# Kernel optimization log

Measured on AMD Instinct MI355X. Metric: run time of the kernel, lower is better.

The kernel has to match this reference:

```python
import jax, jax.numpy as jnp
import numpy as np

B, N, D, H_IMG, W_IMG = 1, 6, 128, 28, 60
HB, WB = 50, 50
HEADS, DH = 4, 32
INNER = HEADS * DH  # 128 == D
Q = HB * WB
NK = N * H_IMG * W_IMG


def _ln(x, w, b, eps=1e-5):
    m = jnp.mean(x, axis=-1, keepdims=True)
    v = jnp.var(x, axis=-1, keepdims=True)
    return (x - m) * jax.lax.rsqrt(v + eps) * w + b


def setup_inputs() -> dict:
    key = jax.random.key(0)
    ks = jax.random.split(key, 20)
    s = 0.02
    inp = {
        "q": jax.random.normal(ks[0], (B, D, HB, WB), jnp.float32),
        "k": jax.random.normal(ks[1], (B, N, D, H_IMG, W_IMG), jnp.float32),
        "v": jax.random.normal(ks[2], (B, N, D, H_IMG, W_IMG), jnp.float32),
        "W_logits": jax.random.uniform(ks[3], (B, Q, NK), jnp.float32),
        "vis_flat": jax.random.randint(ks[4], (B, Q, NK), 0, 2).astype(jnp.int32),
        "skip": jax.random.normal(ks[5], (B, D, HB, WB), jnp.float32),
        # LayerNorm params
        "qn_w": jnp.ones((D,), jnp.float32), "qn_b": jnp.zeros((D,), jnp.float32),
        "kn_w": jnp.ones((D,), jnp.float32), "kn_b": jnp.zeros((D,), jnp.float32),
        "vn_w": jnp.ones((D,), jnp.float32), "vn_b": jnp.zeros((D,), jnp.float32),
        "pre_w": jnp.ones((D,), jnp.float32), "pre_b": jnp.zeros((D,), jnp.float32),
        "post_w": jnp.ones((D,), jnp.float32), "post_b": jnp.zeros((D,), jnp.float32),
        # Linear params, stored [in, out]
        "wq": jax.random.normal(ks[6], (D, INNER), jnp.float32) * s,
        "bq": jnp.zeros((INNER,), jnp.float32),
        "wk": jax.random.normal(ks[7], (D, INNER), jnp.float32) * s,
        "bk": jnp.zeros((INNER,), jnp.float32),
        "wv": jax.random.normal(ks[8], (D, INNER), jnp.float32) * s,
        "bv": jnp.zeros((INNER,), jnp.float32),
        "wp": jax.random.normal(ks[9], (INNER, D), jnp.float32) * s,
        "bp": jnp.zeros((D,), jnp.float32),
        "w1": jax.random.normal(ks[10], (D, 2 * D), jnp.float32) * s,
        "b1": jnp.zeros((2 * D,), jnp.float32),
        "w2": jax.random.normal(ks[11], (2 * D, D), jnp.float32) * s,
        "b2": jnp.zeros((D,), jnp.float32),
    }
    return inp


def reference(q, k, v, W_logits, vis_flat, skip,
              qn_w, qn_b, kn_w, kn_b, vn_w, vn_b, pre_w, pre_b, post_w, post_b,
              wq, bq, wk, bk, wv, bv, wp, bp, w1, b1, w2, b2):
    b, d, Hb, Wb = q.shape
    _, n, _, hi, wi = k.shape
    Qn = Hb * Wb
    # b d H W -> b (H W) d ; b n d h w -> b (n h w) d
    qf = q.reshape(b, d, Qn).transpose(0, 2, 1)
    kf = k.transpose(0, 1, 3, 4, 2).reshape(b, n * hi * wi, d)
    vf = v.transpose(0, 1, 3, 4, 2).reshape(b, n * hi * wi, d)
    qf = _ln(qf, qn_w, qn_b)
    kf = _ln(kf, kn_w, kn_b)
    vf = _ln(vf, vn_w, vn_b)
    qh = (qf @ wq + bq).reshape(b, Qn, HEADS, DH).transpose(0, 2, 1, 3)
    kh = (kf @ wk + bk).reshape(b, -1, HEADS, DH).transpose(0, 2, 1, 3)
    vh = (vf @ wv + bv).reshape(b, -1, HEADS, DH).transpose(0, 2, 1, 3)
    scale = DH ** (-0.5)
    logits = jnp.einsum('bhqd,bhkd->bhqk', qh, kh) * scale  # [b,h,Q,NK]
    neg_inf = jnp.finfo(logits.dtype).min
    logits = jnp.where(vis_flat[:, None] == 0, neg_inf, logits)
    logits = logits * W_logits[:, None]  # multiplicative EAF weighting
    attn = jax.nn.softmax(logits, axis=-1)
    out = jnp.einsum('bhqk,bhkd->bhqd', attn, vh)
    out = out.transpose(0, 2, 1, 3).reshape(b, Qn, INNER)
    out = out @ wp + bp
    z = out + skip.reshape(b, d, Qn).transpose(0, 2, 1)
    z = _ln(z, pre_w, pre_b)
    z = z + (jax.nn.gelu(z @ w1 + b1, approximate=False) @ w2 + b2)
    z = _ln(z, post_w, post_b)
    return z.transpose(0, 2, 1).reshape(b, d, Hb, Wb)
```

## Files before the change

### kernel.cpp

```cpp
#include <hip/hip_runtime.h>
#include <hip/hip_bf16.h>
#include <math.h>

typedef short short8 __attribute__((ext_vector_type(8)));
typedef float floatx4 __attribute__((ext_vector_type(4)));

#define D 128
#define Q 2500
#define QPAD 2560
#define NK 10080
#define NKPAD 10112
#define QSCALE 0.25501268426834347f
#define NEGBIG -3.0e38f

__device__ __forceinline__ unsigned short f2bf(float f) {
    unsigned u = __float_as_uint(f);
    unsigned r = (u + 0x7fffu + ((u >> 16) & 1u)) >> 16;
    return (unsigned short)r;
}

__global__ void ln_kernel(const float* __restrict__ qi, const float* __restrict__ ki,
                          const float* __restrict__ vi,
                          const float* __restrict__ qw, const float* __restrict__ qb,
                          const float* __restrict__ kw, const float* __restrict__ kb,
                          const float* __restrict__ vw, const float* __restrict__ vb,
                          unsigned short* __restrict__ xq, unsigned short* __restrict__ xk,
                          unsigned short* __restrict__ xv) {
    int job = blockIdx.x * 4 + (threadIdx.x >> 6);
    int lane = threadIdx.x & 63;
    const float *g, *b, *a0, *a1;
    unsigned short* dst;
    if (job < Q) {
        int p = job;
        a0 = qi + lane * Q + p; a1 = qi + (lane + 64) * Q + p;
        g = qw; b = qb; dst = xq + p * D;
    } else if (job < Q + NK) {
        int p = job - Q;
        int n = p / 1680; int r = p - n * 1680;
        const float* base = ki + (n * 128) * 1680 + r;
        a0 = base + lane * 1680; a1 = base + (lane + 64) * 1680;
        g = kw; b = kb; dst = xk + p * D;
    } else {
        int p = job - (Q + NK);
        int n = p / 1680; int r = p - n * 1680;
        const float* base = vi + (n * 128) * 1680 + r;
        a0 = base + lane * 1680; a1 = base + (lane + 64) * 1680;
        g = vw; b = vb; dst = xv + p * D;
    }
    float x0 = *a0, x1 = *a1;
    float s = x0 + x1, ss = x0 * x0 + x1 * x1;
    #pragma unroll
    for (int m = 1; m <= 32; m <<= 1) {
        s += __shfl_xor(s, m, 64);
        ss += __shfl_xor(ss, m, 64);
    }
    float mean = s * (1.0f / 128.0f);
    float var = ss * (1.0f / 128.0f) - mean * mean;
    float rstd = rsqrtf(var + 1e-5f);
    dst[lane] = f2bf((x0 - mean) * rstd * g[lane] + b[lane]);
    dst[lane + 64] = f2bf((x1 - mean) * rstd * g[lane + 64] + b[lane + 64]);
}

__global__ __launch_bounds__(256) void proj_kernel(
    const unsigned short* __restrict__ xq, const unsigned short* __restrict__ xk,
    const unsigned short* __restrict__ xv,
    const float* __restrict__ wq, const float* __restrict__ bq,
    const float* __restrict__ wk, const float* __restrict__ bk,
    const float* __restrict__ wv, const float* __restrict__ bv,
    unsigned short* __restrict__ qh, unsigned short* __restrict__ kh,
    unsigned short* __restrict__ vh) {
    int bid = blockIdx.x;
    const unsigned short* src; const float *w, *bias; unsigned short* dst; float scale; int mb;
    if (bid < 40)       { src = xq; w = wq; bias = bq; dst = qh; scale = QSCALE; mb = bid * 64; }
    else if (bid < 198) { src = xk; w = wk; bias = bk; dst = kh; scale = 1.0f;  mb = (bid - 40) * 64; }
    else                { src = xv; w = wv; bias = bv; dst = vh; scale = 1.0f;  mb = (bid - 198) * 64; }
    int wave = threadIdx.x >> 6, lane = threadIdx.x & 63;
    int l15 = lane & 15, quad = lane >> 4;
    int m0 = mb + wave * 16;
    floatx4 acc[8];
    #pragma unroll
    for (int i = 0; i < 8; i++) acc[i] = (floatx4){0.f, 0.f, 0.f, 0.f};
    #pragma unroll
    for (int kf = 0; kf < 4; kf++) {
        short8 A = *(const short8*)(src + (m0 + l15) * D + kf * 32 + quad * 8);
        #pragma unroll
        for (int nt = 0; nt < 8; nt++) {
            short8 B;
            #pragma unroll
            for (int j = 0; j < 8; j++)
                B[j] = (short)f2bf(w[(kf * 32 + quad * 8 + j) * D + nt * 16 + l15]);
            acc[nt] = __builtin_amdgcn_mfma_f32_16x16x32_bf16(A, B, acc[nt], 0, 0, 0);
        }
    }
    #pragma unroll
    for (int nt = 0; nt < 8; nt++) {
        float bb = bias[nt * 16 + l15];
        #pragma unroll
        for (int r = 0; r < 4; r++)
            dst[(m0 + quad * 4 + r) * D + nt * 16 + l15] = f2bf((acc[nt][r] + bb) * scale);
    }
}

__global__ __launch_bounds__(256) void attn_kernel(
    const unsigned short* __restrict__ qh, const unsigned short* __restrict__ kh,
    const unsigned short* __restrict__ vh,
    const float* __restrict__ Wl, const int* __restrict__ vis,
    float* __restrict__ Opart, float* __restrict__ lpart) {
    __shared__ short plds[4 * 2 * 16 * 40];
    int bid = blockIdx.x;
    int split = bid & 7, qt = bid >> 3;
    int h = threadIdx.x >> 6, lane = threadIdx.x & 63;
    int l15 = lane & 15, quad = lane >> 4;
    int qb = qt * 32;
    int kb0 = split * 1280;
    int nch = (split == 7) ? 35 : 40;
    short* pw = plds + h * 1280;

    short8 qA[2];
    #pragma unroll
    for (int s = 0; s < 2; s++)
        qA[s] = *(const short8*)(qh + (qb + s * 16 + l15) * D + h * 32 + quad * 8);

    const float* wrow[8]; const int* vrow[8];
    #pragma unroll
    for (int s = 0; s < 2; s++)
        #pragma unroll
        for (int r = 0; r < 4; r++) {
            int row = qb + s * 16 + quad * 4 + r;
            row = row < Q ? row : (Q - 1);
            wrow[s * 4 + r] = Wl + (size_t)row * NK;
            vrow[s * 4 + r] = vis + (size_t)row * NK;
        }

    const floatx4 zf = {0.f, 0.f, 0.f, 0.f};
    floatx4 O[2][2];
    float lacc[2][4];
    #pragma unroll
    for (int s = 0; s < 2; s++)
        #pragma unroll
        for (int i = 0; i < 4; i++) { lacc[s][i] = 0.f; }
    O[0][0] = zf; O[0][1] = zf; O[1][0] = zf; O[1][1] = zf;

    for (int c = 0; c < nch; c++) {
        int kb = kb0 + c * 32;
        short8 kB0 = *(const short8*)(kh + (kb + l15) * D + h * 32 + quad * 8);
        short8 kB1 = *(const short8*)(kh + (kb + 16 + l15) * D + h * 32 + quad * 8);
        short8 vB0, vB1;
        #pragma unroll
        for (int j = 0; j < 8; j++) {
            int kk = kb + quad * 8 + j;
            vB0[j] = (short)vh[kk * D + h * 32 + l15];
            vB1[j] = (short)vh[kk * D + h * 32 + 16 + l15];
        }
        #pragma unroll
        for (int s = 0; s < 2; s++) {
            floatx4 S0 = __builtin_amdgcn_mfma_f32_16x16x32_bf16(qA[s], kB0, zf, 0, 0, 0);
            floatx4 S1 = __builtin_amdgcn_mfma_f32_16x16x32_bf16(qA[s], kB1, zf, 0, 0, 0);
            #pragma unroll
            for (int r = 0; r < 4; r++) {
                const float* wr = wrow[s * 4 + r];
                const int* vr = vrow[s * 4 + r];
                float w0 = wr[kb + l15], w1 = wr[kb + 16 + l15];
                int v0 = vr[kb + l15], v1 = vr[kb + 16 + l15];
                float L0 = (v0 ? S0[r] : NEGBIG) * w0;
                float L1 = (v1 ? S1[r] : NEGBIG) * w1;
                float p0 = exp2f(L0), p1 = exp2f(L1);
                lacc[s][r] += p0 + p1;
                pw[s * 640 + (quad * 4 + r) * 40 + l15] = (short)f2bf(p0);
                pw[s * 640 + (quad * 4 + r) * 40 + 16 + l15] = (short)f2bf(p1);
            }
        }
        #pragma unroll
        for (int s = 0; s < 2; s++) {
            short8 P = *(const short8*)(pw + s * 640 + l15 * 40 + quad * 8);
            O[s][0] = __builtin_amdgcn_mfma_f32_16x16x32_bf16(P, vB0, O[s][0], 0, 0, 0);
            O[s][1] = __builtin_amdgcn_mfma_f32_16x16x32_bf16(P, vB1, O[s][1], 0, 0, 0);
        }
    }

    #pragma unroll
    for (int s = 0; s < 2; s++)
        #pragma unroll
        for (int r = 0; r < 4; r++) {
            float lv = lacc[s][r];
            lv += __shfl_xor(lv, 1, 64);
            lv += __shfl_xor(lv, 2, 64);
            lv += __shfl_xor(lv, 4, 64);
            lv += __shfl_xor(lv, 8, 64);
            int row = qb + s * 16 + quad * 4 + r;
            if (l15 == 0) lpart[(split * QPAD + row) * 4 + h] = lv;
            float* op = Opart + ((size_t)(split * QPAD + row) * 4 + h) * 32;
            op[l15] = O[s][0][r];
            op[16 + l15] = O[s][1][r];
        }
}

__global__ __launch_bounds__(256) void epi_kernel(
    const float* __restrict__ Opart, const float* __restrict__ lpart,
    const float* __restrict__ wp, const float* __restrict__ bp,
    const float* __restrict__ skip,
    const float* __restrict__ pre_w, const float* __restrict__ pre_b,
    const float* __restrict__ w1, const float* __restrict__ b1,
    const float* __restrict__ w2, const float* __restrict__ b2,
    const float* __restrict__ post_w, const float* __restrict__ post_b,
    float* __restrict__ out) {
    __shared__ __align__(16) char smem[68608];
    short* A1 = (short*)smem;
    short* Z1 = (short*)(smem + 17408);
    short* H1 = (short*)(smem + 34816);
    float* Zout = (float*)smem;

    int qb = blockIdx.x * 64;
    int t = threadIdx.x;
    int wave = t >> 6, lane = t & 63;
    int l15 = lane & 15, quad = lane >> 4;
    int m0 = wave * 16;

    {
        int pl = t >> 2, hh = t & 3;
        int q = qb + pl;
        if (q < Q) {
            float ltot = 0.f;
            #pragma unroll
            for (int s = 0; s < 8; s++) ltot += lpart[(s * QPAD + q) * 4 + hh];
            float inv = 1.0f / fmaxf(ltot, 1e-30f);
            floatx4 acc4[8];
            #pragma unroll
            for (int i = 0; i < 8; i++) acc4[i] = (floatx4){0.f, 0.f, 0.f, 0.f};
            #pragma unroll
            for (int s = 0; s < 8; s++) {
                const floatx4* op = (const floatx4*)(Opart + ((size_t)(s * QPAD + q) * 4 + hh) * 32);
                #pragma unroll
                for (int i = 0; i < 8; i++) acc4[i] += op[i];
            }
            #pragma unroll
            for (int i = 0; i < 8; i++)
                #pragma unroll
                for (int j = 0; j < 4; j++)
                    A1[pl * 136 + hh * 32 + i * 4 + j] = (short)f2bf(acc4[i][j] * inv);
        } else {
            #pragma unroll
            for (int d = 0; d < 32; d++) A1[pl * 136 + hh * 32 + d] = 0;
        }
    }

    floatx4 z[8];
    #pragma unroll
    for (int i = 0; i < 8; i++) z[i] = (floatx4){0.f, 0.f, 0.f, 0.f};
    #pragma unroll
    for (int kf = 0; kf < 4; kf++) {
        short8 A = *(const short8*)(A1 + (m0 + l15) * 136 + kf * 32 + quad * 8);
        #pragma unroll
        for (int nt = 0; nt < 8; nt++) {
            short8 B;
            #pragma unroll
            for (int j = 0; j < 8; j++)
                B[j] = (short)f2bf(wp[(kf * 32 + quad * 8 + j) * D + nt * 16 + l15]);
            z[nt] = __builtin_amdgcn_mfma_f32_16x16x32_bf16(A, B, z[nt], 0, 0, 0);
        }
    }
    float Zv[8][4];
    #pragma unroll
    for (int nt = 0; nt < 8; nt++) {
        int n = nt * 16 + l15;
        float bb = bp[n];
        #pragma unroll
        for (int r = 0; r < 4; r++) {
            int q = qb + m0 + quad * 4 + r;
            int qc = q < Q ? q : (Q - 1);
            Zv[nt][r] = z[nt][r] + bb + skip[n * Q + qc];
        }
    }
    float Zn[8][4];
    {
        #pragma unroll
        for (int r = 0; r < 4; r++) {
            float s1 = 0.f, s2 = 0.f;
            #pragma unroll
            for (int nt = 0; nt < 8; nt++) { s1 += Zv[nt][r]; s2 += Zv[nt][r] * Zv[nt][r]; }
            s1 += __shfl_xor(s1, 1, 64); s2 += __shfl_xor(s2, 1, 64);
            s1 += __shfl_xor(s1, 2, 64); s2 += __shfl_xor(s2, 2, 64);
            s1 += __shfl_xor(s1, 4, 64); s2 += __shfl_xor(s2, 4, 64);
            s1 += __shfl_xor(s1, 8, 64); s2 += __shfl_xor(s2, 8, 64);
            float mean = s1 * (1.0f / 128.0f);
            float var = s2 * (1.0f / 128.0f) - mean * mean;
            float rstd = rsqrtf(var + 1e-5f);
            #pragma unroll
            for (int nt = 0; nt < 8; nt++) Zn[nt][r] = (Zv[nt][r] - mean) * rstd;
        }
        #pragma unroll
        for (int nt = 0; nt < 8; nt++) {
            int n = nt * 16 + l15;
            float g = pre_w[n], be = pre_b[n];
            #pragma unroll
            for (int r = 0; r < 4; r++) {
                Zn[nt][r] = Zn[nt][r] * g + be;
                Z1[(m0 + quad * 4 + r) * 136 + n] = (short)f2bf(Zn[nt][r]);
            }
        }
    }
    {
        floatx4 h2[16];
        #pragma unroll
        for (int i = 0; i < 16; i++) h2[i] = (floatx4){0.f, 0.f, 0.f, 0.f};
        #pragma unroll
        for (int kf = 0; kf < 4; kf++) {
            short8 A = *(const short8*)(Z1 + (m0 + l15) * 136 + kf * 32 + quad * 8);
            #pragma unroll
            for (int nt = 0; nt < 16; nt++) {
                short8 B;
                #pragma unroll
                for (int j = 0; j < 8; j++)
                    B[j] = (short)f2bf(w1[(kf * 32 + quad * 8 + j) * 256 + nt * 16 + l15]);
                h2[nt] = __builtin_amdgcn_mfma_f32_16x16x32_bf16(A, B, h2[nt], 0, 0, 0);
            }
        }
        #pragma unroll
        for (int nt = 0; nt < 16; nt++) {
            int n = nt * 16 + l15;
            float bb = b1[n];
            #pragma unroll
            for (int r = 0; r < 4; r++) {
                float x = h2[nt][r] + bb;
                float gl = 0.5f * x * (1.0f + erff(x * 0.70710678118654752f));
                H1[(m0 + quad * 4 + r) * 264 + n] = (short)f2bf(gl);
            }
        }
    }
    floatx4 o3[8];
    #pragma unroll
    for (int i = 0; i < 8; i++) o3[i] = (floatx4){0.f, 0.f, 0.f, 0.f};
    #pragma unroll
    for (int kf = 0; kf < 8; kf++) {
        short8 A = *(const short8*)(H1 + (m0 + l15) * 264 + kf * 32 + quad * 8);
        #pragma unroll
        for (int nt = 0; nt < 8; nt++) {
            short8 B;
            #pragma unroll
            for (int j = 0; j < 8; j++)
                B[j] = (short)f2bf(w2[(kf * 32 + quad * 8 + j) * D + nt * 16 + l15]);
            o3[nt] = __builtin_amdgcn_mfma_f32_16x16x32_bf16(A, B, o3[nt], 0, 0, 0);
        }
    }
    float Z2[8][4];
    #pragma unroll
    for (int nt = 0; nt < 8; nt++) {
        int n = nt * 16 + l15;
        float bb = b2[n];
        #pragma unroll
        for (int r = 0; r < 4; r++) Z2[nt][r] = Zn[nt][r] + o3[nt][r] + bb;
    }
    float Zo[8][4];
    {
        #pragma unroll
        for (int r = 0; r < 4; r++) {
            float s1 = 0.f, s2 = 0.f;
            #pragma unroll
            for (int nt = 0; nt < 8; nt++) { s1 += Z2[nt][r]; s2 += Z2[nt][r] * Z2[nt][r]; }
            s1 += __shfl_xor(s1, 1, 64); s2 += __shfl_xor(s2, 1, 64);
            s1 += __shfl_xor(s1, 2, 64); s2 += __shfl_xor(s2, 2, 64);
            s1 += __shfl_xor(s1, 4, 64); s2 += __shfl_xor(s2, 4, 64);
            s1 += __shfl_xor(s1, 8, 64); s2 += __shfl_xor(s2, 8, 64);
            float mean = s1 * (1.0f / 128.0f);
            float var = s2 * (1.0f / 128.0f) - mean * mean;
            float rstd = rsqrtf(var + 1e-5f);
            #pragma unroll
            for (int nt = 0; nt < 8; nt++) Zo[nt][r] = (Z2[nt][r] - mean) * rstd;
        }
        #pragma unroll
        for (int nt = 0; nt < 8; nt++) {
            int n = nt * 16 + l15;
            float g = post_w[n], be = post_b[n];
            #pragma unroll
            for (int r = 0; r < 4; r++) Zo[nt][r] = Zo[nt][r] * g + be;
        }
    }
    __syncthreads();
    #pragma unroll
    for (int nt = 0; nt < 8; nt++)
        #pragma unroll
        for (int r = 0; r < 4; r++)
            Zout[(nt * 16 + l15) * 65 + m0 + quad * 4 + r] = Zo[nt][r];
    __syncthreads();
    {
        int pl = t & 63;
        int q = qb + pl;
        if (q < Q) {
            #pragma unroll
            for (int it = 0; it < 32; it++) {
                int n = it * 4 + (t >> 6);
                out[n * Q + q] = Zout[n * 65 + pl];
            }
        }
    }
}

extern "C" void kernel_launch(void* const* d_in, const int* in_sizes, int n_in,
                              void* d_out, int out_size, void* d_ws, size_t ws_size,
                              hipStream_t stream) {
    (void)in_sizes; (void)n_in; (void)out_size; (void)ws_size;
    const float* q      = (const float*)d_in[0];
    const float* k      = (const float*)d_in[1];
    const float* v      = (const float*)d_in[2];
    const float* Wl     = (const float*)d_in[3];
    const int*   vis    = (const int*)  d_in[4];
    const float* skip   = (const float*)d_in[5];
    const float* qn_w   = (const float*)d_in[6];
    const float* qn_b   = (const float*)d_in[7];
    const float* kn_w   = (const float*)d_in[8];
    const float* kn_b   = (const float*)d_in[9];
    const float* vn_w   = (const float*)d_in[10];
    const float* vn_b   = (const float*)d_in[11];
    const float* pre_w  = (const float*)d_in[12];
    const float* pre_b  = (const float*)d_in[13];
    const float* post_w = (const float*)d_in[14];
    const float* post_b = (const float*)d_in[15];
    const float* wq     = (const float*)d_in[16];
    const float* bq     = (const float*)d_in[17];
    const float* wk     = (const float*)d_in[18];
    const float* bk     = (const float*)d_in[19];
    const float* wv     = (const float*)d_in[20];
    const float* bv     = (const float*)d_in[21];
    const float* wp     = (const float*)d_in[22];
    const float* bp     = (const float*)d_in[23];
    const float* w1     = (const float*)d_in[24];
    const float* b1     = (const float*)d_in[25];
    const float* w2     = (const float*)d_in[26];
    const float* b2     = (const float*)d_in[27];
    float* out = (float*)d_out;

    char* ws = (char*)d_ws;
    unsigned short* xq = (unsigned short*)(ws + 0);
    unsigned short* xk = (unsigned short*)(ws + 655360);
    unsigned short* xv = (unsigned short*)(ws + 3244032);
    unsigned short* qh = (unsigned short*)(ws + 5832704);
    unsigned short* kh = (unsigned short*)(ws + 6488064);
    unsigned short* vh = (unsigned short*)(ws + 9076736);
    float* Opart = (float*)(ws + 11665408);
    float* lpart = (float*)(ws + 22151168);

    ln_kernel<<<dim3(5665), dim3(256), 0, stream>>>(q, k, v, qn_w, qn_b, kn_w, kn_b, vn_w, vn_b,
                                                    xq, xk, xv);
    proj_kernel<<<dim3(356), dim3(256), 0, stream>>>(xq, xk, xv, wq, bq, wk, bk, wv, bv,
                                                     qh, kh, vh);
    attn_kernel<<<dim3(632), dim3(256), 0, stream>>>(qh, kh, vh, Wl, vis, Opart, lpart);
    epi_kernel<<<dim3(40), dim3(256), 0, stream>>>(Opart, lpart, wp, bp, skip,
                                                   pre_w, pre_b, w1, b1, w2, b2,
                                                   post_w, post_b, out);
}
```

Baseline: 433.8 us.

## Restructure pipeline: pre-transposed bf16 weights, all-heads attention waves, more splits

A new kernel converts and transposes all weights to bf16 once, so the GEMMs load B fragments as vectors instead of gathering and converting scalars. LayerNorm is rewritten to stage tiles in LDS so global loads are coalesced. V is stored transposed so attention reads it as vectors. Attention now has each wave cover all four heads for 16 queries, which reuses the Wl/vis loads across heads, and the key range is split 35 ways for more blocks. The old epilogue becomes separate linv, combine and MLP kernels, which adds launches and a larger partial-output buffer.

```diff
diff --git a/kernel.cpp b/kernel.cpp
--- a/kernel.cpp
+++ b/kernel.cpp
@@ -10,6 +10,8 @@
 #define QPAD 2560
 #define NK 10080
 #define NKPAD 10112
+#define SPLITS 35
+#define CPS 9
 #define QSCALE 0.25501268426834347f
 #define NEGBIG -3.0e38f
 
@@ -18,63 +20,121 @@
     unsigned r = (u + 0x7fffu + ((u >> 16) & 1u)) >> 16;
     return (unsigned short)r;
 }
-
-__global__ void ln_kernel(const float* __restrict__ qi, const float* __restrict__ ki,
-                          const float* __restrict__ vi,
-                          const float* __restrict__ qw, const float* __restrict__ qb,
-                          const float* __restrict__ kw, const float* __restrict__ kb,
-                          const float* __restrict__ vw, const float* __restrict__ vb,
-                          unsigned short* __restrict__ xq, unsigned short* __restrict__ xk,
-                          unsigned short* __restrict__ xv) {
-    int job = blockIdx.x * 4 + (threadIdx.x >> 6);
-    int lane = threadIdx.x & 63;
-    const float *g, *b, *a0, *a1;
-    unsigned short* dst;
-    if (job < Q) {
-        int p = job;
-        a0 = qi + lane * Q + p; a1 = qi + (lane + 64) * Q + p;
-        g = qw; b = qb; dst = xq + p * D;
-    } else if (job < Q + NK) {
-        int p = job - Q;
-        int n = p / 1680; int r = p - n * 1680;
-        const float* base = ki + (n * 128) * 1680 + r;
-        a0 = base + lane * 1680; a1 = base + (lane + 64) * 1680;
-        g = kw; b = kb; dst = xk + p * D;
+__device__ __forceinline__ unsigned pack2bf(float lo, float hi) {
+    unsigned u0 = __float_as_uint(lo) + 0x8000u;
+    unsigned u1 = __float_as_uint(hi) + 0x8000u;
+    return (u0 >> 16) | (u1 & 0xffff0000u);
+}
+__device__ __forceinline__ float bflo(unsigned u) { return __uint_as_float(u << 16); }
+__device__ __forceinline__ float bfhi(unsigned u) { return __uint_as_float(u & 0xffff0000u); }
+
+__global__ void wcvt_kernel(const float* __restrict__ wq, const float* __restrict__ wk,
+                            const float* __restrict__ wv, const float* __restrict__ wp,
+                            const float* __restrict__ w1, const float* __restrict__ w2,
+                            unsigned short* __restrict__ wqT, unsigned short* __restrict__ wkT,
+                            unsigned short* __restrict__ wvT, unsigned short* __restrict__ wpT,
+                            unsigned short* __restrict__ w1T, unsigned short* __restrict__ w2T) {
+    int idx = blockIdx.x * 256 + threadIdx.x;
+    if (idx < 49152) {
+        int m = idx >> 14;
+        int local = idx & 16383;
+        int n = local >> 7, kk = local & 127;
+        const float* w = (m == 0) ? wq : ((m == 1) ? wk : wv);
+        unsigned short* o = (m == 0) ? wqT : ((m == 1) ? wkT : wvT);
+        o[local] = f2bf(w[kk * 128 + n]);
+    } else if (idx < 65536) {
+        int local = idx - 49152;
+        int n = local >> 7, kk = local & 127;
+        int b = kk >> 5, j = kk & 31;
+        int ko = b * 32 + ((j & 1) ? 16 + (j >> 1) : (j >> 1));
+        wpT[local] = f2bf(wp[ko * 128 + n]);
+    } else if (idx < 98304) {
+        int local = idx - 65536;
+        int n = local >> 7, kk = local & 127;
+        w1T[local] = f2bf(w1[kk * 256 + n]);
     } else {
-        int p = job - (Q + NK);
-        int n = p / 1680; int r = p - n * 1680;
-        const float* base = vi + (n * 128) * 1680 + r;
-        a0 = base + lane * 1680; a1 = base + (lane + 64) * 1680;
-        g = vw; b = vb; dst = xv + p * D;
-    }
-    float x0 = *a0, x1 = *a1;
-    float s = x0 + x1, ss = x0 * x0 + x1 * x1;
-    #pragma unroll
-    for (int m = 1; m <= 32; m <<= 1) {
-        s += __shfl_xor(s, m, 64);
-        ss += __shfl_xor(ss, m, 64);
-    }
+        int local = idx - 98304;
+        int n = local >> 8, kk = local & 255;
+        w2T[local] = f2bf(w2[kk * 128 + n]);
+    }
+}
+
+__global__ __launch_bounds__(256) void ln_kernel(
+    const float* __restrict__ qi, const float* __restrict__ ki, const float* __restrict__ vi,
+    const float* __restrict__ qw, const float* __restrict__ qb,
+    const float* __restrict__ kw, const float* __restrict__ kb,
+    const float* __restrict__ vw, const float* __restrict__ vb,
+    unsigned short* __restrict__ xq, unsigned short* __restrict__ xk,
+    unsigned short* __restrict__ xv) {
+    __shared__ float lds[16 * 132];
+    int bid = blockIdx.x, t = threadIdx.x;
+    const float* src; unsigned short* dst; const float *g, *b;
+    int S, valid;
+    if (bid < 157) {
+        int p0 = bid * 16;
+        src = qi + p0; S = Q; dst = xq + p0 * D; g = qw; b = qb;
+        valid = Q - p0; if (valid > 16) valid = 16;
+    } else if (bid < 787) {
+        int tt = bid - 157;
+        int n = tt / 105, r = (tt - n * 105) * 16;
+        src = ki + (size_t)(n * 128) * 1680 + r; S = 1680;
+        dst = xk + (n * 1680 + r) * D; g = kw; b = kb; valid = 16;
+    } else {
+        int tt = bid - 787;
+        int n = tt / 105, r = (tt - n * 105) * 16;
+        src = vi + (size_t)(n * 128) * 1680 + r; S = 1680;
+        dst = xv + (n * 1680 + r) * D; g = vw; b = vb; valid = 16;
+    }
+    int c4 = t & 3, d = t >> 2;
+    floatx4 fa = {0.f, 0.f, 0.f, 0.f}, fb = {0.f, 0.f, 0.f, 0.f};
+    if (c4 * 4 < valid) {
+        fa = *(const floatx4*)(src + d * S + c4 * 4);
+        fb = *(const floatx4*)(src + (d + 64) * S + c4 * 4);
+    }
+    #pragma unroll
+    for (int j = 0; j < 4; j++) {
+        lds[(c4 * 4 + j) * 132 + d] = fa[j];
+        lds[(c4 * 4 + j) * 132 + d + 64] = fb[j];
+    }
+    __syncthreads();
+    int lane = t & 63, wv = t >> 6;
+    int pos = wv * 4 + (lane >> 4), l15 = lane & 15;
+    floatx4 xa = *(const floatx4*)(&lds[pos * 132 + l15 * 8]);
+    floatx4 xb = *(const floatx4*)(&lds[pos * 132 + l15 * 8 + 4]);
+    float s = 0.f, ss = 0.f;
+    #pragma unroll
+    for (int j = 0; j < 4; j++) { s += xa[j] + xb[j]; ss += xa[j] * xa[j] + xb[j] * xb[j]; }
+    #pragma unroll
+    for (int m = 1; m <= 8; m <<= 1) { s += __shfl_xor(s, m, 64); ss += __shfl_xor(ss, m, 64); }
     float mean = s * (1.0f / 128.0f);
     float var = ss * (1.0f / 128.0f) - mean * mean;
     float rstd = rsqrtf(var + 1e-5f);
-    dst[lane] = f2bf((x0 - mean) * rstd * g[lane] + b[lane]);
-    dst[lane + 64] = f2bf((x1 - mean) * rstd * g[lane + 64] + b[lane + 64]);
+    floatx4 g0 = *(const floatx4*)(g + l15 * 8), g1 = *(const floatx4*)(g + l15 * 8 + 4);
+    floatx4 b0 = *(const floatx4*)(b + l15 * 8), b1 = *(const floatx4*)(b + l15 * 8 + 4);
+    short8 o;
+    #pragma unroll
+    for (int j = 0; j < 4; j++) {
+        o[j] = (short)f2bf((xa[j] - mean) * rstd * g0[j] + b0[j]);
+        o[4 + j] = (short)f2bf((xb[j] - mean) * rstd * g1[j] + b1[j]);
+    }
+    if (pos < valid) *(short8*)(dst + pos * D + l15 * 8) = o;
 }
 
 __global__ __launch_bounds__(256) void proj_kernel(
     const unsigned short* __restrict__ xq, const unsigned short* __restrict__ xk,
     const unsigned short* __restrict__ xv,
-    const float* __restrict__ wq, const float* __restrict__ bq,
-    const float* __restrict__ wk, const float* __restrict__ bk,
-    const float* __restrict__ wv, const float* __restrict__ bv,
+    const unsigned short* __restrict__ wqT, const unsigned short* __restrict__ wkT,
+    const unsigned short* __restrict__ wvT,
+    const float* __restrict__ bq, const float* __restrict__ bk, const float* __restrict__ bv,
     unsigned short* __restrict__ qh, unsigned short* __restrict__ kh,
-    unsigned short* __restrict__ vh) {
+    unsigned short* __restrict__ vhT) {
+    __shared__ short vlds[128 * 72];
     int bid = blockIdx.x;
-    const unsigned short* src; const float *w, *bias; unsigned short* dst; float scale; int mb;
-    if (bid < 40)       { src = xq; w = wq; bias = bq; dst = qh; scale = QSCALE; mb = bid * 64; }
-    else if (bid < 198) { src = xk; w = wk; bias = bk; dst = kh; scale = 1.0f;  mb = (bid - 40) * 64; }
-    else                { src = xv; w = wv; bias = bv; dst = vh; scale = 1.0f;  mb = (bid - 198) * 64; }
-    int wave = threadIdx.x >> 6, lane = threadIdx.x & 63;
+    const unsigned short *src, *wT; const float* bias; int mb, mode; float scale;
+    if (bid < 40)       { mode = 0; src = xq; wT = wqT; bias = bq; mb = bid * 64; scale = QSCALE; }
+    else if (bid < 198) { mode = 1; src = xk; wT = wkT; bias = bk; mb = (bid - 40) * 64; scale = 1.0f; }
+    else                { mode = 2; src = xv; wT = wvT; bias = bv; mb = (bid - 198) * 64; scale = 1.0f; }
+    int t = threadIdx.x, wave = t >> 6, lane = t & 63;
     int l15 = lane & 15, quad = lane >> 4;
     int m0 = mb + wave * 16;
     floatx4 acc[8];
@@ -85,178 +145,183 @@
         short8 A = *(const short8*)(src + (m0 + l15) * D + kf * 32 + quad * 8);
         #pragma unroll
         for (int nt = 0; nt < 8; nt++) {
-            short8 B;
-            #pragma unroll
-            for (int j = 0; j < 8; j++)
-                B[j] = (short)f2bf(w[(kf * 32 + quad * 8 + j) * D + nt * 16 + l15]);
-            acc[nt] = __builtin_amdgcn_mfma_f32_16x16x32_bf16(A, B, acc[nt], 0, 0, 0);
-        }
-    }
-    #pragma unroll
-    for (int nt = 0; nt < 8; nt++) {
-        float bb = bias[nt * 16 + l15];
-        #pragma unroll
-        for (int r = 0; r < 4; r++)
-            dst[(m0 + quad * 4 + r) * D + nt * 16 + l15] = f2bf((acc[nt][r] + bb) * scale);
+            short8 Bv = *(const short8*)(wT + (nt * 16 + l15) * D + kf * 32 + quad * 8);
+            acc[nt] = __builtin_amdgcn_mfma_f32_16x16x32_bf16(A, Bv, acc[nt], 0, 0, 0);
+        }
+    }
+    if (mode != 2) {
+        unsigned short* dst = (mode == 0) ? qh : kh;
+        #pragma unroll
+        for (int nt = 0; nt < 8; nt++) {
+            float bb = bias[nt * 16 + l15];
+            #pragma unroll
+            for (int r = 0; r < 4; r++)
+                dst[(m0 + quad * 4 + r) * D + nt * 16 + l15] = f2bf((acc[nt][r] + bb) * scale);
+        }
+    } else {
+        #pragma unroll
+        for (int nt = 0; nt < 8; nt++) {
+            float bb = bias[nt * 16 + l15];
+            #pragma unroll
+            for (int r = 0; r < 4; r++)
+                vlds[(nt * 16 + l15) * 72 + (wave * 16 + quad * 4 + r)] =
+                    (short)f2bf(acc[nt][r] + bb);
+        }
+        __syncthreads();
+        int pr = t & 31, dd = t >> 5;
+        int sub = pr >> 4, i = pr & 15;
+        #pragma unroll
+        for (int pass = 0; pass < 16; pass++) {
+            int d = pass * 8 + dd;
+            unsigned lo = (unsigned short)vlds[d * 72 + sub * 32 + i];
+            unsigned hi = (unsigned short)vlds[d * 72 + sub * 32 + 16 + i];
+            *(unsigned*)(vhT + (size_t)d * NKPAD + mb + sub * 32 + 2 * i) = lo | (hi << 16);
+        }
     }
 }
 
 __global__ __launch_bounds__(256) void attn_kernel(
     const unsigned short* __restrict__ qh, const unsigned short* __restrict__ kh,
-    const unsigned short* __restrict__ vh,
+    const unsigned short* __restrict__ vhT,
     const float* __restrict__ Wl, const int* __restrict__ vis,
-    float* __restrict__ Opart, float* __restrict__ lpart) {
-    __shared__ short plds[4 * 2 * 16 * 40];
+    unsigned* __restrict__ OpartU, float* __restrict__ lpart) {
+    __shared__ unsigned pP[4 * 4 * 16 * 20];
     int bid = blockIdx.x;
-    int split = bid & 7, qt = bid >> 3;
-    int h = threadIdx.x >> 6, lane = threadIdx.x & 63;
+    int split = bid % SPLITS, qt = bid / SPLITS;
+    int t = threadIdx.x, wave = t >> 6, lane = t & 63;
     int l15 = lane & 15, quad = lane >> 4;
-    int qb = qt * 32;
-    int kb0 = split * 1280;
-    int nch = (split == 7) ? 35 : 40;
-    short* pw = plds + h * 1280;
-
-    short8 qA[2];
-    #pragma unroll
-    for (int s = 0; s < 2; s++)
-        qA[s] = *(const short8*)(qh + (qb + s * 16 + l15) * D + h * 32 + quad * 8);
-
-    const float* wrow[8]; const int* vrow[8];
-    #pragma unroll
-    for (int s = 0; s < 2; s++)
+    int qb = qt * 64 + wave * 16;
+    int k00 = split * (CPS * 32);
+    unsigned* pw = pP + wave * 1280;
+
+    short8 qA[4];
+    #pragma unroll
+    for (int h = 0; h < 4; h++)
+        qA[h] = *(const short8*)(qh + (qb + l15) * D + h * 32 + quad * 8);
+
+    const float* wrow[4]; const int* vrow[4];
+    #pragma unroll
+    for (int r = 0; r < 4; r++) {
+        int row = qb + quad * 4 + r;
+        row = row < Q ? row : (Q - 1);
+        wrow[r] = Wl + (size_t)row * NK;
+        vrow[r] = vis + (size_t)row * NK;
+    }
+
+    const floatx4 zf = {0.f, 0.f, 0.f, 0.f};
+    floatx4 O[4][2];
+    float lacc[4][4];
+    #pragma unroll
+    for (int h = 0; h < 4; h++) {
+        O[h][0] = zf; O[h][1] = zf;
+        #pragma unroll
+        for (int r = 0; r < 4; r++) lacc[h][r] = 0.f;
+    }
+
+    #pragma unroll 1
+    for (int c = 0; c < CPS; c++) {
+        int k0 = k00 + c * 32;
+        float w0[4], w1[4]; int msk0[4], msk1[4];
         #pragma unroll
         for (int r = 0; r < 4; r++) {
-            int row = qb + s * 16 + quad * 4 + r;
-            row = row < Q ? row : (Q - 1);
-            wrow[s * 4 + r] = Wl + (size_t)row * NK;
-            vrow[s * 4 + r] = vis + (size_t)row * NK;
-        }
-
-    const floatx4 zf = {0.f, 0.f, 0.f, 0.f};
-    floatx4 O[2][2];
-    float lacc[2][4];
-    #pragma unroll
-    for (int s = 0; s < 2; s++)
-        #pragma unroll
-        for (int i = 0; i < 4; i++) { lacc[s][i] = 0.f; }
-    O[0][0] = zf; O[0][1] = zf; O[1][0] = zf; O[1][1] = zf;
-
-    for (int c = 0; c < nch; c++) {
-        int kb = kb0 + c * 32;
-        short8 kB0 = *(const short8*)(kh + (kb + l15) * D + h * 32 + quad * 8);
-        short8 kB1 = *(const short8*)(kh + (kb + 16 + l15) * D + h * 32 + quad * 8);
-        short8 vB0, vB1;
-        #pragma unroll
-        for (int j = 0; j < 8; j++) {
-            int kk = kb + quad * 8 + j;
-            vB0[j] = (short)vh[kk * D + h * 32 + l15];
-            vB1[j] = (short)vh[kk * D + h * 32 + 16 + l15];
-        }
-        #pragma unroll
-        for (int s = 0; s < 2; s++) {
-            floatx4 S0 = __builtin_amdgcn_mfma_f32_16x16x32_bf16(qA[s], kB0, zf, 0, 0, 0);
-            floatx4 S1 = __builtin_amdgcn_mfma_f32_16x16x32_bf16(qA[s], kB1, zf, 0, 0, 0);
+            w0[r] = wrow[r][k0 + l15];
+            w1[r] = wrow[r][k0 + 16 + l15];
+            msk0[r] = vrow[r][k0 + l15];
+            msk1[r] = vrow[r][k0 + 16 + l15];
+        }
+        #pragma unroll
+        for (int h = 0; h < 4; h++) {
+            short8 kB0 = *(const short8*)(kh + (k0 + l15) * D + h * 32 + quad * 8);
+            short8 kB1 = *(const short8*)(kh + (k0 + 16 + l15) * D + h * 32 + quad * 8);
+            floatx4 S0 = __builtin_amdgcn_mfma_f32_16x16x32_bf16(qA[h], kB0, zf, 0, 0, 0);
+            floatx4 S1 = __builtin_amdgcn_mfma_f32_16x16x32_bf16(qA[h], kB1, zf, 0, 0, 0);
             #pragma unroll
             for (int r = 0; r < 4; r++) {
-                const float* wr = wrow[s * 4 + r];
-                const int* vr = vrow[s * 4 + r];
-                float w0 = wr[kb + l15], w1 = wr[kb + 16 + l15];
-                int v0 = vr[kb + l15], v1 = vr[kb + 16 + l15];
-                float L0 = (v0 ? S0[r] : NEGBIG) * w0;
-                float L1 = (v1 ? S1[r] : NEGBIG) * w1;
+                float L0 = (msk0[r] ? S0[r] : NEGBIG) * w0[r];
+                float L1 = (msk1[r] ? S1[r] : NEGBIG) * w1[r];
                 float p0 = exp2f(L0), p1 = exp2f(L1);
-                lacc[s][r] += p0 + p1;
-                pw[s * 640 + (quad * 4 + r) * 40 + l15] = (short)f2bf(p0);
-                pw[s * 640 + (quad * 4 + r) * 40 + 16 + l15] = (short)f2bf(p1);
+                lacc[h][r] += p0 + p1;
+                pw[h * 320 + (quad * 4 + r) * 20 + l15] = pack2bf(p0, p1);
             }
         }
         #pragma unroll
-        for (int s = 0; s < 2; s++) {
-            short8 P = *(const short8*)(pw + s * 640 + l15 * 40 + quad * 8);
-            O[s][0] = __builtin_amdgcn_mfma_f32_16x16x32_bf16(P, vB0, O[s][0], 0, 0, 0);
-            O[s][1] = __builtin_amdgcn_mfma_f32_16x16x32_bf16(P, vB1, O[s][1], 0, 0, 0);
-        }
-    }
-
-    #pragma unroll
-    for (int s = 0; s < 2; s++)
+        for (int h = 0; h < 4; h++) {
+            short8 P = *(const short8*)(pw + h * 320 + l15 * 20 + quad * 4);
+            short8 vB0 = *(const short8*)(vhT + (size_t)(h * 32 + l15) * NKPAD + k0 + quad * 8);
+            short8 vB1 = *(const short8*)(vhT + (size_t)(h * 32 + 16 + l15) * NKPAD + k0 + quad * 8);
+            O[h][0] = __builtin_amdgcn_mfma_f32_16x16x32_bf16(P, vB0, O[h][0], 0, 0, 0);
+            O[h][1] = __builtin_amdgcn_mfma_f32_16x16x32_bf16(P, vB1, O[h][1], 0, 0, 0);
+        }
+    }
+
+    #pragma unroll
+    for (int h = 0; h < 4; h++)
         #pragma unroll
         for (int r = 0; r < 4; r++) {
-            float lv = lacc[s][r];
+            float lv = lacc[h][r];
             lv += __shfl_xor(lv, 1, 64);
             lv += __shfl_xor(lv, 2, 64);
             lv += __shfl_xor(lv, 4, 64);
             lv += __shfl_xor(lv, 8, 64);
-            int row = qb + s * 16 + quad * 4 + r;
-            if (l15 == 0) lpart[(split * QPAD + row) * 4 + h] = lv;
-            float* op = Opart + ((size_t)(split * QPAD + row) * 4 + h) * 32;
-            op[l15] = O[s][0][r];
-            op[16 + l15] = O[s][1][r];
-        }
-}
-
-__global__ __launch_bounds__(256) void epi_kernel(
-    const float* __restrict__ Opart, const float* __restrict__ lpart,
-    const float* __restrict__ wp, const float* __restrict__ bp,
-    const float* __restrict__ skip,
+            int row = qb + quad * 4 + r;
+            int base = (split * QPAD + row) * 4 + h;
+            if (l15 == 0) lpart[base] = lv;
+            OpartU[base * 16 + l15] = pack2bf(O[h][0][r], O[h][1][r]);
+        }
+}
+
+__global__ void linv_kernel(const float* __restrict__ lpart, float* __restrict__ linv) {
+    int i = blockIdx.x * 256 + threadIdx.x;
+    float s = 0.f;
+    #pragma unroll 1
+    for (int sp = 0; sp < SPLITS; sp++) s += lpart[sp * QPAD * 4 + i];
+    linv[i] = 1.0f / fmaxf(s, 1e-30f);
+}
+
+__global__ void combine_kernel(const unsigned* __restrict__ OpartU,
+                               const float* __restrict__ linv,
+                               unsigned* __restrict__ A1u) {
+    int idx = blockIdx.x * 256 + threadIdx.x;
+    float lo = 0.f, hi = 0.f;
+    #pragma unroll 1
+    for (int sp = 0; sp < SPLITS; sp++) {
+        unsigned u = OpartU[(size_t)sp * (QPAD * 64) + idx];
+        lo += bflo(u);
+        hi += bfhi(u);
+    }
+    int q = idx >> 6, t6 = idx & 63;
+    float inv = linv[q * 4 + (t6 >> 4)];
+    A1u[idx] = pack2bf(lo * inv, hi * inv);
+}
+
+__global__ __launch_bounds__(256) void mlp_kernel(
+    const unsigned short* __restrict__ A1s, const unsigned short* __restrict__ wpT,
+    const float* __restrict__ bp, const float* __restrict__ skip,
     const float* __restrict__ pre_w, const float* __restrict__ pre_b,
-    const float* __restrict__ w1, const float* __restrict__ b1,
-    const float* __restrict__ w2, const float* __restrict__ b2,
+    const unsigned short* __restrict__ w1T, const float* __restrict__ b1,
+    const unsigned short* __restrict__ w2T, const float* __restrict__ b2,
     const float* __restrict__ post_w, const float* __restrict__ post_b,
     float* __restrict__ out) {
-    __shared__ __align__(16) char smem[68608];
-    short* A1 = (short*)smem;
-    short* Z1 = (short*)(smem + 17408);
-    short* H1 = (short*)(smem + 34816);
+    __shared__ __align__(16) char smem[51200];
+    short* Z1 = (short*)smem;
+    short* H1 = (short*)(smem + 17408);
     float* Zout = (float*)smem;
 
     int qb = blockIdx.x * 64;
-    int t = threadIdx.x;
-    int wave = t >> 6, lane = t & 63;
+    int t = threadIdx.x, wave = t >> 6, lane = t & 63;
     int l15 = lane & 15, quad = lane >> 4;
     int m0 = wave * 16;
 
-    {
-        int pl = t >> 2, hh = t & 3;
-        int q = qb + pl;
-        if (q < Q) {
-            float ltot = 0.f;
-            #pragma unroll
-            for (int s = 0; s < 8; s++) ltot += lpart[(s * QPAD + q) * 4 + hh];
-            float inv = 1.0f / fmaxf(ltot, 1e-30f);
-            floatx4 acc4[8];
-            #pragma unroll
-            for (int i = 0; i < 8; i++) acc4[i] = (floatx4){0.f, 0.f, 0.f, 0.f};
-            #pragma unroll
-            for (int s = 0; s < 8; s++) {
-                const floatx4* op = (const floatx4*)(Opart + ((size_t)(s * QPAD + q) * 4 + hh) * 32);
-                #pragma unroll
-                for (int i = 0; i < 8; i++) acc4[i] += op[i];
-            }
-            #pragma unroll
-            for (int i = 0; i < 8; i++)
-                #pragma unroll
-                for (int j = 0; j < 4; j++)
-                    A1[pl * 136 + hh * 32 + i * 4 + j] = (short)f2bf(acc4[i][j] * inv);
-        } else {
-            #pragma unroll
-            for (int d = 0; d < 32; d++) A1[pl * 136 + hh * 32 + d] = 0;
-        }
-    }
-
     floatx4 z[8];
     #pragma unroll
     for (int i = 0; i < 8; i++) z[i] = (floatx4){0.f, 0.f, 0.f, 0.f};
     #pragma unroll
     for (int kf = 0; kf < 4; kf++) {
-        short8 A = *(const short8*)(A1 + (m0 + l15) * 136 + kf * 32 + quad * 8);
-        #pragma unroll
-        for (int nt = 0; nt < 8; nt++) {
-            short8 B;
-            #pragma unroll
-            for (int j = 0; j < 8; j++)
-                B[j] = (short)f2bf(wp[(kf * 32 + quad * 8 + j) * D + nt * 16 + l15]);
-            z[nt] = __builtin_amdgcn_mfma_f32_16x16x32_bf16(A, B, z[nt], 0, 0, 0);
+        short8 A = *(const short8*)(A1s + (qb + m0 + l15) * D + kf * 32 + quad * 8);
+        #pragma unroll
+        for (int nt = 0; nt < 8; nt++) {
+            short8 Bv = *(const short8*)(wpT + (nt * 16 + l15) * D + kf * 32 + quad * 8);
+            z[nt] = __builtin_amdgcn_mfma_f32_16x16x32_bf16(A, Bv, z[nt], 0, 0, 0);
         }
     }
     float Zv[8][4];
@@ -278,10 +343,8 @@
             float s1 = 0.f, s2 = 0.f;
             #pragma unroll
             for (int nt = 0; nt < 8; nt++) { s1 += Zv[nt][r]; s2 += Zv[nt][r] * Zv[nt][r]; }
-            s1 += __shfl_xor(s1, 1, 64); s2 += __shfl_xor(s2, 1, 64);
-            s1 += __shfl_xor(s1, 2, 64); s2 += __shfl_xor(s2, 2, 64);
-            s1 += __shfl_xor(s1, 4, 64); s2 += __shfl_xor(s2, 4, 64);
-            s1 += __shfl_xor(s1, 8, 64); s2 += __shfl_xor(s2, 8, 64);
+            #pragma unroll
+            for (int m = 1; m <= 8; m <<= 1) { s1 += __shfl_xor(s1, m, 64); s2 += __shfl_xor(s2, m, 64); }
             float mean = s1 * (1.0f / 128.0f);
             float var = s2 * (1.0f / 128.0f) - mean * mean;
             float rstd = rsqrtf(var + 1e-5f);
@@ -308,11 +371,8 @@
             short8 A = *(const short8*)(Z1 + (m0 + l15) * 136 + kf * 32 + quad * 8);
             #pragma unroll
             for (int nt = 0; nt < 16; nt++) {
-                short8 B;
-                #pragma unroll
-                for (int j = 0; j < 8; j++)
-                    B[j] = (short)f2bf(w1[(kf * 32 + quad * 8 + j) * 256 + nt * 16 + l15]);
-                h2[nt] = __builtin_amdgcn_mfma_f32_16x16x32_bf16(A, B, h2[nt], 0, 0, 0);
+                short8 Bv = *(const short8*)(w1T + (nt * 16 + l15) * D + kf * 32 + quad * 8);
+                h2[nt] = __builtin_amdgcn_mfma_f32_16x16x32_bf16(A, Bv, h2[nt], 0, 0, 0);
             }
         }
         #pragma unroll
@@ -335,11 +395,8 @@
         short8 A = *(const short8*)(H1 + (m0 + l15) * 264 + kf * 32 + quad * 8);
         #pragma unroll
         for (int nt = 0; nt < 8; nt++) {
-            short8 B;
-            #pragma unroll
-            for (int j = 0; j < 8; j++)
-                B[j] = (short)f2bf(w2[(kf * 32 + quad * 8 + j) * D + nt * 16 + l15]);
-            o3[nt] = __builtin_amdgcn_mfma_f32_16x16x32_bf16(A, B, o3[nt], 0, 0, 0);
+            short8 Bv = *(const short8*)(w2T + (nt * 16 + l15) * 256 + kf * 32 + quad * 8);
+            o3[nt] = __builtin_amdgcn_mfma_f32_16x16x32_bf16(A, Bv, o3[nt], 0, 0, 0);
         }
     }
     float Z2[8][4];
@@ -357,10 +414,8 @@
             float s1 = 0.f, s2 = 0.f;
             #pragma unroll
             for (int nt = 0; nt < 8; nt++) { s1 += Z2[nt][r]; s2 += Z2[nt][r] * Z2[nt][r]; }
-            s1 += __shfl_xor(s1, 1, 64); s2 += __shfl_xor(s2, 1, 64);
-            s1 += __shfl_xor(s1, 2, 64); s2 += __shfl_xor(s2, 2, 64);
-            s1 += __shfl_xor(s1, 4, 64); s2 += __shfl_xor(s2, 4, 64);
-            s1 += __shfl_xor(s1, 8, 64); s2 += __shfl_xor(s2, 8, 64);
+            #pragma unroll
+            for (int m = 1; m <= 8; m <<= 1) { s1 += __shfl_xor(s1, m, 64); s2 += __shfl_xor(s2, m, 64); }
             float mean = s1 * (1.0f / 128.0f);
             float var = s2 * (1.0f / 128.0f) - mean * mean;
             float rstd = rsqrtf(var + 1e-5f);
@@ -430,21 +485,33 @@
     float* out = (float*)d_out;
 
     char* ws = (char*)d_ws;
-    unsigned short* xq = (unsigned short*)(ws + 0);
-    unsigned short* xk = (unsigned short*)(ws + 655360);
-    unsigned short* xv = (unsigned short*)(ws + 3244032);
-    unsigned short* qh = (unsigned short*)(ws + 5832704);
-    unsigned short* kh = (unsigned short*)(ws + 6488064);
-    unsigned short* vh = (unsigned short*)(ws + 9076736);
-    float* Opart = (float*)(ws + 11665408);
-    float* lpart = (float*)(ws + 22151168);
-
-    ln_kernel<<<dim3(5665), dim3(256), 0, stream>>>(q, k, v, qn_w, qn_b, kn_w, kn_b, vn_w, vn_b,
+    unsigned short* xq  = (unsigned short*)(ws + 0);
+    unsigned short* xk  = (unsigned short*)(ws + 655360);
+    unsigned short* xv  = (unsigned short*)(ws + 3244032);
+    unsigned short* qh  = (unsigned short*)(ws + 5832704);
+    unsigned short* kh  = (unsigned short*)(ws + 6488064);
+    unsigned short* vhT = (unsigned short*)(ws + 9076736);
+    unsigned short* wqT = (unsigned short*)(ws + 11665408);
+    unsigned short* wkT = (unsigned short*)(ws + 11698176);
+    unsigned short* wvT = (unsigned short*)(ws + 11730944);
+    unsigned short* wpT = (unsigned short*)(ws + 11763712);
+    unsigned short* w1T = (unsigned short*)(ws + 11796480);
+    unsigned short* w2T = (unsigned short*)(ws + 11862016);
+    unsigned* OpartU    = (unsigned*)(ws + 11927552);
+    float* lpart        = (float*)(ws + 34865152);
+    float* linv         = (float*)(ws + 36298752);
+    unsigned* A1u       = (unsigned*)(ws + 36339712);
+
+    wcvt_kernel<<<dim3(512), dim3(256), 0, stream>>>(wq, wk, wv, wp, w1, w2,
+                                                     wqT, wkT, wvT, wpT, w1T, w2T);
+    ln_kernel<<<dim3(1417), dim3(256), 0, stream>>>(q, k, v, qn_w, qn_b, kn_w, kn_b, vn_w, vn_b,
                                                     xq, xk, xv);
-    proj_kernel<<<dim3(356), dim3(256), 0, stream>>>(xq, xk, xv, wq, bq, wk, bk, wv, bv,
-                                                     qh, kh, vh);
-    attn_kernel<<<dim3(632), dim3(256), 0, stream>>>(qh, kh, vh, Wl, vis, Opart, lpart);
-    epi_kernel<<<dim3(40), dim3(256), 0, stream>>>(Opart, lpart, wp, bp, skip,
-                                                   pre_w, pre_b, w1, b1, w2, b2,
+    proj_kernel<<<dim3(356), dim3(256), 0, stream>>>(xq, xk, xv, wqT, wkT, wvT, bq, bk, bv,
+                                                     qh, kh, vhT);
+    attn_kernel<<<dim3(40 * SPLITS), dim3(256), 0, stream>>>(qh, kh, vhT, Wl, vis, OpartU, lpart);
+    linv_kernel<<<dim3(40), dim3(256), 0, stream>>>(lpart, linv);
+    combine_kernel<<<dim3(640), dim3(256), 0, stream>>>(OpartU, linv, A1u);
+    mlp_kernel<<<dim3(40), dim3(256), 0, stream>>>((const unsigned short*)A1u, wpT, bp, skip,
+                                                   pre_w, pre_b, w1T, b1, w2T, b2,
                                                    post_w, post_b, out);
 }
```

Result: no change. 426.1 us (-1.8%).
